# Performance work log

Hardware: AMD Instinct MI355X
Metric: run time of the kernel (lower is better)

## Reference

```python
import jax, jax.numpy as jnp
import numpy as np

B = 8            # batch
P = 28           # patch grid (224 / 8 for wide_resnet50_2 layer2)
D = 1536         # 512 (layer2) + 1024 (layer3) channels
M = 50000        # memory bank size
NUM_NEIGHBORS = 9
INPUT_SIZE = 224
SIGMA = 4.0
KSIZE = 2 * int(4.0 * SIGMA + 0.5) + 1  # 33, anomalib GaussianBlur2d convention


def setup_inputs() -> dict:
    key = jax.random.key(0)
    k1, k2 = jax.random.split(key)
    embedding = jax.random.normal(k1, (B * P * P, D), dtype=jnp.float32)
    memory_bank = jax.random.normal(k2, (M, D), dtype=jnp.float32)
    return {"embedding": embedding, "memory_bank": memory_bank}


def euclidean_dist(x, y):
    x_norm = jnp.sum(x * x, axis=-1, keepdims=True)
    y_norm = jnp.sum(y * y, axis=-1, keepdims=True)
    res = x_norm - 2.0 * jnp.matmul(x, jnp.swapaxes(y, -2, -1)) + jnp.swapaxes(y_norm, -2, -1)
    return jnp.sqrt(jnp.clip(res, 0.0, None))


def gaussian_kernel1d(ksize, sigma):
    x = jnp.arange(ksize, dtype=jnp.float32) - (ksize - 1) / 2.0
    g = jnp.exp(-(x * x) / (2.0 * sigma * sigma))
    return g / jnp.sum(g)


def gaussian_blur(img):
    # separable depthwise gaussian blur with reflect padding (kornia/anomalib style), img: [B,1,H,W]
    g = gaussian_kernel1d(KSIZE, SIGMA)
    pad = KSIZE // 2
    img = jnp.pad(img, ((0, 0), (0, 0), (pad, pad), (pad, pad)), mode='reflect')
    kh = g.reshape(1, 1, KSIZE, 1)
    kw = g.reshape(1, 1, 1, KSIZE)
    dn = ('NCHW', 'OIHW', 'NCHW')
    img = jax.lax.conv_general_dilated(img, kh, (1, 1), 'VALID', dimension_numbers=dn)
    img = jax.lax.conv_general_dilated(img, kw, (1, 1), 'VALID', dimension_numbers=dn)
    return img


def reference(embedding, memory_bank):
    # ---- nearest_neighbors(embedding, n_neighbors=1) ----
    dists = euclidean_dist(embedding, memory_bank)            # [B*P*P, M]
    patch_scores = jnp.min(dists, axis=1).reshape(B, P * P)   # [B, P*P]
    locations = jnp.argmin(dists, axis=1).reshape(B, P * P)   # [B, P*P]

    # ---- compute_anomaly_score (num_neighbors = 9) ----
    batch_idx = jnp.arange(B)
    max_patches = jnp.argmax(patch_scores, axis=1)                       # [B]
    feats = embedding.reshape(B, P * P, D)
    max_patches_features = feats[batch_idx, max_patches]                 # [B, D]
    score = patch_scores[batch_idx, max_patches]                         # [B]
    nn_index = locations[batch_idx, max_patches]                         # [B]
    nn_sample = memory_bank[nn_index]                                    # [B, D]
    d2 = euclidean_dist(nn_sample, memory_bank)                          # [B, M]
    _, support_samples = jax.lax.top_k(-d2, NUM_NEIGHBORS)               # smallest-k, ascending
    supp_feats = memory_bank[support_samples]                            # [B, K, D]
    d3 = euclidean_dist(max_patches_features[:, None, :], supp_feats)    # [B, 1, K]
    weights = (1.0 - jax.nn.softmax(d3[:, 0, :], axis=1))[:, 0]          # [B]
    pred_score = weights * score                                         # [B]

    # ---- anomaly map: bilinear upsample (align_corners=False) + gaussian blur ----
    pmap = patch_scores.reshape(B, 1, P, P)
    amap = jax.image.resize(pmap, (B, 1, INPUT_SIZE, INPUT_SIZE), method='bilinear')
    anomaly_map = gaussian_blur(amap)                                    # [B,1,224,224]
    return anomaly_map, pred_score
```

## Files before the change

kernel.cpp:

```cpp
#include <hip/hip_runtime.h>
#include <cstdint>
#include <cstddef>

#define DDIM 1536
#define NROWS 6272
#define NROWPAD 6400
#define MBANK 50000
#define NCOLPAD 50176
#define NRT 49
#define NCT 392
#define NSLOT (NCT * 2)
#define NKT 24
#define NB 8
#define PP 784
#define HW 224
#define KS 33
#define PAD 16

typedef __attribute__((ext_vector_type(4))) int int4v;
typedef __attribute__((ext_vector_type(4))) float floatx4;

__device__ __forceinline__ unsigned long long u64min(unsigned long long a, unsigned long long b) {
  return a < b ? a : b;
}

__global__ __launch_bounds__(256) void convnorm8_kernel(const float* __restrict__ in,
                                                        signed char* __restrict__ out,
                                                        float* __restrict__ norm,
                                                        int valid_rows, int total_rows) {
  int row = blockIdx.x * 4 + (threadIdx.x >> 6);
  int lane = threadIdx.x & 63;
  if (row >= total_rows) return;
  int* dst = (int*)(out + (size_t)row * DDIM);
  float s = 0.f;
  if (row < valid_rows) {
    const float4* src = (const float4*)(in + (size_t)row * DDIM);
#pragma unroll
    for (int i = 0; i < 6; i++) {
      int d = lane + i * 64;
      float4 v = src[d];
      s = fmaf(v.x, v.x, s); s = fmaf(v.y, v.y, s);
      s = fmaf(v.z, v.z, s); s = fmaf(v.w, v.w, s);
      int q0 = min(max((int)rintf(v.x * 16.f), -127), 127);
      int q1 = min(max((int)rintf(v.y * 16.f), -127), 127);
      int q2 = min(max((int)rintf(v.z * 16.f), -127), 127);
      int q3 = min(max((int)rintf(v.w * 16.f), -127), 127);
      dst[d] = (q0 & 255) | ((q1 & 255) << 8) | ((q2 & 255) << 16) | ((q3 & 255) << 24);
    }
  } else {
#pragma unroll
    for (int i = 0; i < 6; i++) dst[lane + i * 64] = 0;
  }
  for (int off = 32; off; off >>= 1) s += __shfl_down(s, off, 64);
  if (lane == 0) norm[row] = s;
}

__global__ __launch_bounds__(256) void rownorm_kernel(const float* __restrict__ x,
                                                      float* __restrict__ out, int rows) {
  int row = blockIdx.x;
  if (row >= rows) return;
  const float4* p4 = (const float4*)(x + (size_t)row * DDIM);
  float s = 0.f;
  for (int d = threadIdx.x; d < DDIM / 4; d += 256) {
    float4 v = p4[d];
    s = fmaf(v.x, v.x, s); s = fmaf(v.y, v.y, s);
    s = fmaf(v.z, v.z, s); s = fmaf(v.w, v.w, s);
  }
  for (int off = 32; off; off >>= 1) s += __shfl_down(s, off, 64);
  __shared__ float ls[4];
  int wid = threadIdx.x >> 6, lane = threadIdx.x & 63;
  if (lane == 0) ls[wid] = s;
  __syncthreads();
  if (threadIdx.x == 0) out[row] = ls[0] + ls[1] + ls[2] + ls[3];
}

__global__ void init_u64_kernel(unsigned long long* p, int n) {
  int i = blockIdx.x * 256 + threadIdx.x;
  if (i < n) p[i] = ~0ull;
}

__global__ __launch_bounds__(256, 4) void mindist_mfma_kernel(
    const signed char* __restrict__ Ah, const signed char* __restrict__ Bh,
    const float* __restrict__ xnorm, const float* __restrict__ ynorm,
    unsigned long long* __restrict__ cand) {
  __shared__ char smem[32768];

  const int t = threadIdx.x;
  const int lane = t & 63, wid = t >> 6;
  const int wm = wid >> 1, wn = wid & 1;
  const int l15 = lane & 15, g = lane >> 4;

  const int wg = (blockIdx.x & 7) * 2401 + (blockIdx.x >> 3);
  const int rt = wg / NCT, ct = wg % NCT;
  const int row0 = rt * 128;
  const int c0 = ct * 128;

  const int ck = ((g ^ ((l15 >> 1) & 3)) << 4);
  const int aBase = wm * 4096 + l15 * 64;
  const int bBase = 16384 + wn * 4096 + l15 * 64;

  const int cl = (t & 3) ^ ((t >> 3) & 3);
  const signed char* paBase = Ah + (size_t)(row0 + (t >> 2)) * DDIM + cl * 16;
  const signed char* pbBase = Bh + (size_t)(c0 + (t >> 2)) * DDIM + cl * 16;

#define STAGE_KT(kt, d)                                                                  \
  {                                                                                      \
    _Pragma("unroll") for (int j = 0; j < 2; j++) {                                      \
      __builtin_amdgcn_global_load_lds(                                                  \
          (const __attribute__((address_space(1))) void*)(paBase +                       \
              (size_t)(j * 64) * DDIM + (size_t)(kt) * 64),                              \
          (__attribute__((address_space(3))) void*)(smem + (d) * 8192 + j * 4096 +       \
                                                    wid * 1024),                         \
          16, 0, 0);                                                                     \
    }                                                                                    \
    _Pragma("unroll") for (int j = 0; j < 2; j++) {                                      \
      __builtin_amdgcn_global_load_lds(                                                  \
          (const __attribute__((address_space(1))) void*)(pbBase +                       \
              (size_t)(j * 64) * DDIM + (size_t)(kt) * 64),                              \
          (__attribute__((address_space(3))) void*)(smem + 16384 + (d) * 8192 +          \
                                                    j * 4096 + wid * 1024),              \
          16, 0, 0);                                                                     \
    }                                                                                    \
  }

  int4v acc[4][4];
  int4v zz = {0, 0, 0, 0};
#pragma unroll
  for (int mi = 0; mi < 4; mi++)
#pragma unroll
    for (int nf = 0; nf < 4; nf++) acc[mi][nf] = zz;

  STAGE_KT(0, 0);
  STAGE_KT(1, 1);

  for (int kt = 0; kt < NKT; ++kt) {
    const int d = kt & 1;
    if (kt < NKT - 1) {
      asm volatile("s_waitcnt vmcnt(4)" ::: "memory");
    } else {
      asm volatile("s_waitcnt vmcnt(0)" ::: "memory");
    }
    __builtin_amdgcn_sched_barrier(0);
    __builtin_amdgcn_s_barrier();
    __builtin_amdgcn_sched_barrier(0);

    const char* sA = smem + d * 8192 + aBase;
    const char* sB = smem + d * 8192 + bBase;

    int4v ra[4], rb[4];
#pragma unroll
    for (int mi = 0; mi < 4; mi++) ra[mi] = *(const int4v*)(sA + mi * 1024 + ck);
#pragma unroll
    for (int nf = 0; nf < 4; nf++) rb[nf] = *(const int4v*)(sB + nf * 1024 + ck);
    __builtin_amdgcn_s_setprio(1);
#pragma unroll
    for (int mi = 0; mi < 4; mi++)
#pragma unroll
      for (int nf = 0; nf < 4; nf++)
        acc[mi][nf] = __builtin_amdgcn_mfma_i32_16x16x64_i8(ra[mi], rb[nf],
                                                            acc[mi][nf], 0, 0, 0);
    __builtin_amdgcn_s_setprio(0);
    __builtin_amdgcn_sched_barrier(0);
    __builtin_amdgcn_s_barrier();
    __builtin_amdgcn_sched_barrier(0);
    if (kt < NKT - 2) STAGE_KT(kt + 2, d);
  }
#undef STAGE_KT

  float yn[4];
  int colv[4];
#pragma unroll
  for (int nf = 0; nf < 4; nf++) {
    int col = c0 + wn * 64 + nf * 16 + l15;
    colv[nf] = col;
    yn[nf] = (col < MBANK) ? ynorm[col] : 0.f;
  }
#pragma unroll
  for (int mi = 0; mi < 4; mi++) {
    int rowb = row0 + wm * 64 + mi * 16 + g * 4;
#pragma unroll
    for (int q = 0; q < 4; q++) {
      float xnq = xnorm[rowb + q];
      unsigned long long best = ~0ull;
#pragma unroll
      for (int nf = 0; nf < 4; nf++) {
        if (colv[nf] < MBANK) {
          float dsq = fmaxf(xnq + yn[nf] - (float)acc[mi][nf][q] * 0.0078125f, 0.f);
          unsigned long long pk =
              ((unsigned long long)__float_as_uint(dsq) << 32) | (unsigned)colv[nf];
          best = u64min(best, pk);
        }
      }
#pragma unroll
      for (int mask = 1; mask <= 8; mask <<= 1)
        best = u64min(best, __shfl_xor(best, mask, 64));
      if (l15 == 0 && rowb + q < NROWS)
        cand[(size_t)(rowb + q) * NSLOT + ct * 2 + wn] = best;
    }
  }
}

__global__ __launch_bounds__(256) void rerank_kernel(
    const float* __restrict__ emb, const float* __restrict__ mem,
    const float* __restrict__ xnorm, const float* __restrict__ ynorm,
    const unsigned long long* __restrict__ cand, float* __restrict__ ps,
    int* __restrict__ loc) {
  int row = blockIdx.x, t = threadIdx.x;
  int lane = t & 63, wave = t >> 6;
  __shared__ unsigned long long lred[4];
  __shared__ int glist[64];
  __shared__ int gcount;
  __shared__ float gmin;
  const unsigned long long* crow = cand + (size_t)row * NSLOT;
  unsigned long long mn = ~0ull;
  for (int i = t; i < NSLOT; i += 256) mn = u64min(mn, crow[i]);
  for (int off = 32; off; off >>= 1) {
    unsigned long long o = __shfl_down(mn, off, 64);
    mn = u64min(mn, o);
  }
  if (lane == 0) lred[wave] = mn;
  if (t == 0) gcount = 0;
  __syncthreads();
  if (t == 0) {
    unsigned long long m0 = lred[0];
    for (int w = 1; w < 4; w++) m0 = u64min(m0, lred[w]);
    gmin = __uint_as_float((unsigned)(m0 >> 32));
  }
  __syncthreads();
  float gate = gmin + 14.0f;
  for (int i = t; i < NSLOT; i += 256) {
    unsigned long long v = crow[i];
    float dq = __uint_as_float((unsigned)(v >> 32));
    if (dq <= gate) {
      int idx = atomicAdd(&gcount, 1);
      if (idx < 64) glist[idx] = (int)(v & 0xffffffffu);
    }
  }
  __syncthreads();
  int ng = min(gcount, 64);
  float xnv = xnorm[row];
  const float4* xp = (const float4*)(emb + (size_t)row * DDIM);
  unsigned long long best = ~0ull;
  for (int gi = wave; gi < ng; gi += 4) {
    int col = glist[gi];
    const float4* yp = (const float4*)(mem + (size_t)col * DDIM);
    float s = 0.f;
    for (int d4 = lane; d4 < DDIM / 4; d4 += 64) {
      float4 a = xp[d4], b = yp[d4];
      s = fmaf(a.x, b.x, s); s = fmaf(a.y, b.y, s);
      s = fmaf(a.z, b.z, s); s = fmaf(a.w, b.w, s);
    }
    for (int off = 32; off; off >>= 1) s += __shfl_down(s, off, 64);
    if (lane == 0) {
      float dsq = fmaxf(xnv + ynorm[col] - 2.f * s, 0.f);
      unsigned long long pk =
          ((unsigned long long)__float_as_uint(dsq) << 32) | (unsigned)col;
      best = u64min(best, pk);
    }
  }
  if (lane == 0) lred[wave] = best;
  __syncthreads();
  if (t == 0) {
    unsigned long long b = lred[0];
    for (int w = 1; w < 4; w++) b = u64min(b, lred[w]);
    ps[row] = sqrtf(__uint_as_float((unsigned)(b >> 32)));
    loc[row] = (int)(b & 0xffffffffu);
  }
}

#define BM 128
#define BN 128
#define DKC 16
#define FCSPLIT 16
#define FCT ((MBANK + BN - 1) / BN)
#define FCPB ((FCT + FCSPLIT - 1) / FCSPLIT)

__global__ __launch_bounds__(256) void mindist_kernel(
    const float* __restrict__ A, const float* __restrict__ Bm,
    const float* __restrict__ xnorm, const float* __restrict__ ynorm,
    unsigned long long* __restrict__ best) {
  __shared__ float Asf[DKC][BM];
  __shared__ float Bsf[DKC][BN];
  int t = threadIdx.x;
  int tx = t & 15, ty = t >> 4;
  int row0 = blockIdx.x * BM;
  int rloc[8], cloc[8];
#pragma unroll
  for (int i = 0; i < 4; i++) {
    rloc[i] = ty * 4 + i; rloc[i + 4] = 64 + ty * 4 + i;
    cloc[i] = tx * 4 + i; cloc[i + 4] = 64 + tx * 4 + i;
  }
  float xnv[8];
#pragma unroll
  for (int i = 0; i < 8; i++) xnv[i] = xnorm[row0 + rloc[i]];
  unsigned long long bestr[8];
#pragma unroll
  for (int i = 0; i < 8; i++) bestr[i] = ~0ull;
  int ct_begin = blockIdx.y * FCPB;
  int ct_end = ct_begin + FCPB; if (ct_end > FCT) ct_end = FCT;
  for (int ct = ct_begin; ct < ct_end; ++ct) {
    int c0 = ct * BN;
    float acc[8][8];
#pragma unroll
    for (int i = 0; i < 8; i++)
#pragma unroll
      for (int j = 0; j < 8; j++) acc[i][j] = 0.f;
    for (int dk = 0; dk < DDIM; dk += DKC) {
#pragma unroll
      for (int s = 0; s < 2; ++s) {
        int q = t + s * 256;
        int r = q >> 2, c4 = q & 3;
        float4 va = *(const float4*)(A + (size_t)(row0 + r) * DDIM + dk + c4 * 4);
        Asf[c4 * 4 + 0][r] = va.x; Asf[c4 * 4 + 1][r] = va.y;
        Asf[c4 * 4 + 2][r] = va.z; Asf[c4 * 4 + 3][r] = va.w;
        int col = c0 + r;
        float4 vb = make_float4(0.f, 0.f, 0.f, 0.f);
        if (col < MBANK) vb = *(const float4*)(Bm + (size_t)col * DDIM + dk + c4 * 4);
        Bsf[c4 * 4 + 0][r] = vb.x; Bsf[c4 * 4 + 1][r] = vb.y;
        Bsf[c4 * 4 + 2][r] = vb.z; Bsf[c4 * 4 + 3][r] = vb.w;
      }
      __syncthreads();
#pragma unroll
      for (int k = 0; k < DKC; k++) {
        float4 a0 = *(const float4*)&Asf[k][ty * 4];
        float4 a1 = *(const float4*)&Asf[k][64 + ty * 4];
        float4 b0 = *(const float4*)&Bsf[k][tx * 4];
        float4 b1 = *(const float4*)&Bsf[k][64 + tx * 4];
        float av[8] = {a0.x, a0.y, a0.z, a0.w, a1.x, a1.y, a1.z, a1.w};
        float bv[8] = {b0.x, b0.y, b0.z, b0.w, b1.x, b1.y, b1.z, b1.w};
#pragma unroll
        for (int i = 0; i < 8; i++)
#pragma unroll
          for (int j = 0; j < 8; j++) acc[i][j] = fmaf(av[i], bv[j], acc[i][j]);
      }
      __syncthreads();
    }
#pragma unroll
    for (int j = 0; j < 8; j++) {
      int col = c0 + cloc[j];
      if (col < MBANK) {
        float yn = ynorm[col];
#pragma unroll
        for (int i = 0; i < 8; i++) {
          float dsq = fmaxf(xnv[i] + yn - 2.f * acc[i][j], 0.f);
          unsigned long long pk =
              ((unsigned long long)__float_as_uint(dsq) << 32) | (unsigned)col;
          if (pk < bestr[i]) bestr[i] = pk;
        }
      }
    }
  }
#pragma unroll
  for (int i = 0; i < 8; i++) atomicMin(&best[row0 + rloc[i]], bestr[i]);
}

__global__ void unpack_kernel(const unsigned long long* __restrict__ best,
                              float* __restrict__ ps, int* __restrict__ loc) {
  int i = blockIdx.x * 256 + threadIdx.x;
  if (i >= NROWS) return;
  unsigned long long v = best[i];
  ps[i] = sqrtf(__uint_as_float((unsigned)(v >> 32)));
  loc[i] = (int)(v & 0xffffffffu);
}

__global__ __launch_bounds__(256) void argmax_kernel(const float* __restrict__ ps,
                                                     const int* __restrict__ loc,
                                                     float* __restrict__ bscore,
                                                     int* __restrict__ bfrow,
                                                     int* __restrict__ bnn) {
  int b = blockIdx.x, t = threadIdx.x;
  unsigned long long bp = 0;
  for (int p = t; p < PP; p += 256) {
    unsigned long long pk = ((unsigned long long)__float_as_uint(ps[b * PP + p]) << 32) |
                            (unsigned)(0xffffffffu - (unsigned)p);
    if (pk > bp) bp = pk;
  }
  for (int off = 32; off; off >>= 1) {
    unsigned long long o = __shfl_down(bp, off, 64);
    if (o > bp) bp = o;
  }
  __shared__ unsigned long long ls[4];
  int wid = t >> 6, lane = t & 63;
  if (lane == 0) ls[wid] = bp;
  __syncthreads();
  if (t == 0) {
    for (int w = 1; w < 4; w++) if (ls[w] > ls[0]) ls[0] = ls[w];
    unsigned p = 0xffffffffu - (unsigned)(ls[0] & 0xffffffffu);
    bscore[b] = __uint_as_float((unsigned)(ls[0] >> 32));
    bfrow[b] = b * PP + (int)p;
    bnn[b] = loc[b * PP + (int)p];
  }
}

__global__ __launch_bounds__(256) void d2_kernel(const float* __restrict__ mem,
                                                 const float* __restrict__ ynorm,
                                                 const int* __restrict__ bnn,
                                                 float* __restrict__ d2) {
  __shared__ float nn8[NB][DDIM];
  __shared__ float nnorm[NB];
  for (int e = threadIdx.x; e < NB * DDIM; e += 256) {
    int b = e / DDIM, d = e % DDIM;
    nn8[b][d] = mem[(size_t)bnn[b] * DDIM + d];
  }
  if (threadIdx.x < NB) nnorm[threadIdx.x] = ynorm[bnn[threadIdx.x]];
  __syncthreads();
  int wid = threadIdx.x >> 6, lane = threadIdx.x & 63;
  int gw = blockIdx.x * 4 + wid;
  int nw = gridDim.x * 4;
  for (int m = gw; m < MBANK; m += nw) {
    const float4* mp4 = (const float4*)(mem + (size_t)m * DDIM);
    float acc[NB];
#pragma unroll
    for (int b = 0; b < NB; b++) acc[b] = 0.f;
    for (int d4 = lane; d4 < DDIM / 4; d4 += 64) {
      float4 v = mp4[d4];
#pragma unroll
      for (int b = 0; b < NB; b++) {
        float4 w = *(const float4*)&nn8[b][d4 * 4];
        acc[b] = fmaf(v.x, w.x, acc[b]); acc[b] = fmaf(v.y, w.y, acc[b]);
        acc[b] = fmaf(v.z, w.z, acc[b]); acc[b] = fmaf(v.w, w.w, acc[b]);
      }
    }
    float yn = ynorm[m];
#pragma unroll
    for (int b = 0; b < NB; b++) {
      float r = acc[b];
      for (int off = 32; off; off >>= 1) r += __shfl_down(r, off, 64);
      if (lane == 0) d2[(size_t)b * MBANK + m] = sqrtf(fmaxf(nnorm[b] + yn - 2.f * r, 0.f));
    }
  }
}

__global__ __launch_bounds__(256) void topk_kernel(
    const float* __restrict__ emb, const float* __restrict__ mem,
    const float* __restrict__ xnorm, const float* __restrict__ ynorm,
    const float* __restrict__ d2, const float* __restrict__ bscore,
    const int* __restrict__ bfrow, float* __restrict__ pred) {
  int b = blockIdx.x, t = threadIdx.x;
  __shared__ unsigned long long ls9[256][9];
  __shared__ float fred[4];
  __shared__ int supp[9];
  __shared__ float d3s[9];
  const float* row = d2 + (size_t)b * MBANK;
  unsigned long long a0 = ~0ull, a1 = ~0ull, a2 = ~0ull, a3 = ~0ull, a4 = ~0ull,
                     a5 = ~0ull, a6 = ~0ull, a7 = ~0ull, a8 = ~0ull;
  for (int m = t; m < MBANK; m += 256) {
    unsigned long long pk = ((unsigned long long)__float_as_uint(row[m]) << 32) | (unsigned)m;
    if (pk < a8) {
      a8 = pk;
      unsigned long long tv;
#define CSWP(x, y) if (y < x) { tv = x; x = y; y = tv; }
      CSWP(a7, a8) CSWP(a6, a7) CSWP(a5, a6) CSWP(a4, a5)
      CSWP(a3, a4) CSWP(a2, a3) CSWP(a1, a2) CSWP(a0, a1)
#undef CSWP
    }
  }
  ls9[t][0] = a0; ls9[t][1] = a1; ls9[t][2] = a2; ls9[t][3] = a3; ls9[t][4] = a4;
  ls9[t][5] = a5; ls9[t][6] = a6; ls9[t][7] = a7; ls9[t][8] = a8;
  __syncthreads();
  for (int s = 128; s >= 1; s >>= 1) {
    if (t < s) {
      unsigned long long outv[9];
      int i = 0, j = 0;
#pragma unroll
      for (int k = 0; k < 9; k++) {
        unsigned long long x = ls9[t][i], y = ls9[t + s][j];
        if (x <= y) { outv[k] = x; i++; } else { outv[k] = y; j++; }
      }
#pragma unroll
      for (int k = 0; k < 9; k++) ls9[t][k] = outv[k];
    }
    __syncthreads();
  }
  if (t < 9) supp[t] = (int)(ls9[0][t] & 0xffffffffu);
  __syncthreads();
  int frow = bfrow[b];
  const float* x = emb + (size_t)frow * DDIM;
  float xnv = xnorm[frow];
  for (int k = 0; k < 9; k++) {
    const float* y = mem + (size_t)supp[k] * DDIM;
    float s = 0.f;
    for (int d = t; d < DDIM; d += 256) s = fmaf(x[d], y[d], s);
    for (int off = 32; off; off >>= 1) s += __shfl_down(s, off, 64);
    if ((t & 63) == 0) fred[t >> 6] = s;
    __syncthreads();
    if (t == 0) {
      float dot = fred[0] + fred[1] + fred[2] + fred[3];
      d3s[k] = sqrtf(fmaxf(xnv - 2.f * dot + ynorm[supp[k]], 0.f));
    }
    __syncthreads();
  }
  if (t == 0) {
    float mx = d3s[0];
    for (int k = 1; k < 9; k++) mx = fmaxf(mx, d3s[k]);
    float sum = 0.f;
    for (int k = 0; k < 9; k++) sum += expf(d3s[k] - mx);
    float w = 1.f - expf(d3s[0] - mx) / sum;
    pred[b] = w * bscore[b];
  }
}

__global__ void gauss_kernel(float* __restrict__ g) {
  __shared__ float tmp[KS];
  int t = threadIdx.x;
  if (t < KS) {
    float x = (float)t - (float)(KS - 1) * 0.5f;
    tmp[t] = __expf(-(x * x) / 32.0f);
  }
  __syncthreads();
  if (t == 0) {
    float s = 0.f;
    for (int j = 0; j < KS; j++) s += tmp[j];
    for (int j = 0; j < KS; j++) g[j] = tmp[j] / s;
  }
}

__global__ __launch_bounds__(256) void resize_kernel(const float* __restrict__ ps,
                                                     float* __restrict__ out) {
  int idx = blockIdx.x * 256 + threadIdx.x;
  if (idx >= NB * HW * HW) return;
  int x = idx % HW, y = (idx / HW) % HW, b = idx / (HW * HW);
  float sx = (x + 0.5f) * 0.125f - 0.5f;
  float sy = (y + 0.5f) * 0.125f - 0.5f;
  int x0 = (int)floorf(sx), y0 = (int)floorf(sy);
  float fx = sx - x0, fy = sy - y0;
  int x0c = min(max(x0, 0), 27), x1c = min(max(x0 + 1, 0), 27);
  int y0c = min(max(y0, 0), 27), y1c = min(max(y0 + 1, 0), 27);
  const float* p = ps + b * PP;
  float v00 = p[y0c * 28 + x0c], v01 = p[y0c * 28 + x1c];
  float v10 = p[y1c * 28 + x0c], v11 = p[y1c * 28 + x1c];
  out[idx] = v00 * (1.f - fy) * (1.f - fx) + v01 * (1.f - fy) * fx +
             v10 * fy * (1.f - fx) + v11 * fy * fx;
}

__device__ __forceinline__ int reflect224(int i) {
  if (i < 0) i = -i;
  if (i > 223) i = 446 - i;
  return i;
}

__global__ __launch_bounds__(256) void blurv_kernel(const float* __restrict__ in,
                                                    const float* __restrict__ g,
                                                    float* __restrict__ out) {
  __shared__ float gk[KS];
  if (threadIdx.x < KS) gk[threadIdx.x] = g[threadIdx.x];
  __syncthreads();
  int idx = blockIdx.x * 256 + threadIdx.x;
  if (idx >= NB * HW * HW) return;
  int x = idx % HW, y = (idx / HW) % HW, b = idx / (HW * HW);
  const float* base = in + (size_t)b * HW * HW;
  float s = 0.f;
#pragma unroll
  for (int j = 0; j < KS; j++) {
    int yy = reflect224(y - PAD + j);
    s = fmaf(gk[j], base[yy * HW + x], s);
  }
  out[idx] = s;
}

__global__ __launch_bounds__(256) void blurh_kernel(const float* __restrict__ in,
                                                    const float* __restrict__ g,
                                                    float* __restrict__ out) {
  __shared__ float gk[KS];
  if (threadIdx.x < KS) gk[threadIdx.x] = g[threadIdx.x];
  __syncthreads();
  int idx = blockIdx.x * 256 + threadIdx.x;
  if (idx >= NB * HW * HW) return;
  int x = idx % HW, y = (idx / HW) % HW, b = idx / (HW * HW);
  const float* base = in + (size_t)b * HW * HW;
  float s = 0.f;
#pragma unroll
  for (int j = 0; j < KS; j++) {
    int xx = reflect224(x - PAD + j);
    s = fmaf(gk[j], base[y * HW + xx], s);
  }
  out[idx] = s;
}

extern "C" void kernel_launch(void* const* d_in, const int* in_sizes, int n_in,
                              void* d_out, int out_size, void* d_ws, size_t ws_size,
                              hipStream_t stream) {
  const float* emb = (const float*)d_in[0];
  const float* mem = (const float*)d_in[1];
  float* out = (float*)d_out;

  char* ws = (char*)d_ws;
  size_t off = 0;
  auto alloc = [&](size_t bytes) -> void* {
    void* p = ws + off;
    off += (bytes + 255) & ~(size_t)255;
    return p;
  };
  float* ynorm = (float*)alloc((size_t)NCOLPAD * 4);
  float* xnorm = (float*)alloc((size_t)NROWPAD * 4);
  unsigned long long* cand =
      (unsigned long long*)alloc((size_t)NROWS * NSLOT * 8);
  float* ps = (float*)alloc(NROWS * 4);
  int* loc = (int*)alloc(NROWS * 4);
  float* bscore = (float*)alloc(NB * 4);
  int* bfrow = (int*)alloc(NB * 4);
  int* bnn = (int*)alloc(NB * 4);
  float* d2 = (float*)alloc((size_t)NB * MBANK * 4);
  float* g = (float*)alloc(KS * 4);
  float* rsz = (float*)alloc((size_t)NB * HW * HW * 4);
  float* tmp = (float*)alloc((size_t)NB * HW * HW * 4);
  signed char* emb_q = (signed char*)alloc((size_t)NROWPAD * DDIM);
  signed char* mem_q = (signed char*)alloc((size_t)NCOLPAD * DDIM);
  size_t full_need = off;

  bool fast = (ws_size >= full_need);

  if (fast) {
    convnorm8_kernel<<<NCOLPAD / 4, 256, 0, stream>>>(mem, mem_q, ynorm, MBANK, NCOLPAD);
    convnorm8_kernel<<<NROWPAD / 4, 256, 0, stream>>>(emb, emb_q, xnorm, NROWS, NROWPAD);
    mindist_mfma_kernel<<<NRT * NCT, 256, 0, stream>>>(emb_q, mem_q, xnorm, ynorm, cand);
    rerank_kernel<<<NROWS, 256, 0, stream>>>(emb, mem, xnorm, ynorm, cand, ps, loc);
    argmax_kernel<<<NB, 256, 0, stream>>>(ps, loc, bscore, bfrow, bnn);
  } else {
    rownorm_kernel<<<MBANK, 256, 0, stream>>>(mem, ynorm, MBANK);
    rownorm_kernel<<<NROWS, 256, 0, stream>>>(emb, xnorm, NROWS);
    unsigned long long* best = cand;
    init_u64_kernel<<<(NROWS + 255) / 256, 256, 0, stream>>>(best, NROWS);
    mindist_kernel<<<dim3(NROWS / BM, FCSPLIT), 256, 0, stream>>>(emb, mem, xnorm, ynorm,
                                                                  best);
    unpack_kernel<<<(NROWS + 255) / 256, 256, 0, stream>>>(best, ps, loc);
    argmax_kernel<<<NB, 256, 0, stream>>>(ps, loc, bscore, bfrow, bnn);
  }

  d2_kernel<<<1200, 256, 0, stream>>>(mem, ynorm, bnn, d2);
  topk_kernel<<<NB, 256, 0, stream>>>(emb, mem, xnorm, ynorm, d2, bscore, bfrow,
                                      out + (size_t)NB * HW * HW);
  gauss_kernel<<<1, 64, 0, stream>>>(g);
  resize_kernel<<<(NB * HW * HW + 255) / 256, 256, 0, stream>>>(ps, rsz);
  blurv_kernel<<<(NB * HW * HW + 255) / 256, 256, 0, stream>>>(rsz, g, tmp);
  blurh_kernel<<<(NB * HW * HW + 255) / 256, 256, 0, stream>>>(tmp, g, out);
}
```

Baseline: 1.012 ms.

## Fold resize and blur into a 224x28 linear operator; merge conversion kernels

Replaces the bilinear resize and the two separable blur passes with one precomputed 224x28 weight matrix that combines interpolation, reflect padding and the Gaussian. Each batch image is then produced as W·P·Wᵀ by a single block working in shared memory. This removes three full-resolution intermediate passes and several launches. The memory-bank and embedding int8 conversion kernels are also merged into a single launch. The trade-off is only 8 blocks for the anomaly map, so little GPU parallelism, with a serial wprep kernel ahead of it.

```diff
diff --git a/kernel.cpp b/kernel.cpp
--- a/kernel.cpp
+++ b/kernel.cpp
@@ -24,21 +24,44 @@
   return a < b ? a : b;
 }
 
-__global__ __launch_bounds__(256) void convnorm8_kernel(const float* __restrict__ in,
-                                                        signed char* __restrict__ out,
-                                                        float* __restrict__ norm,
-                                                        int valid_rows, int total_rows) {
+__device__ __forceinline__ int reflect224(int i) {
+  if (i < 0) i = -i;
+  if (i > 223) i = 446 - i;
+  return i;
+}
+
+__global__ __launch_bounds__(256) void convnorm_both_kernel(
+    const float* __restrict__ mem, const float* __restrict__ emb,
+    signed char* __restrict__ mem_q, signed char* __restrict__ emb_q,
+    float* __restrict__ ynorm, float* __restrict__ xnorm) {
   int row = blockIdx.x * 4 + (threadIdx.x >> 6);
   int lane = threadIdx.x & 63;
-  if (row >= total_rows) return;
-  int* dst = (int*)(out + (size_t)row * DDIM);
+  const float* src;
+  int* dst;
+  float* norm;
+  bool valid;
+  int r;
+  if (row < NCOLPAD) {
+    r = row;
+    src = mem + (size_t)r * DDIM;
+    dst = (int*)(mem_q + (size_t)r * DDIM);
+    norm = ynorm + r;
+    valid = (r < MBANK);
+  } else {
+    r = row - NCOLPAD;
+    if (r >= NROWPAD) return;
+    src = emb + (size_t)r * DDIM;
+    dst = (int*)(emb_q + (size_t)r * DDIM);
+    norm = xnorm + r;
+    valid = (r < NROWS);
+  }
   float s = 0.f;
-  if (row < valid_rows) {
-    const float4* src = (const float4*)(in + (size_t)row * DDIM);
+  if (valid) {
+    const float4* s4 = (const float4*)src;
 #pragma unroll
     for (int i = 0; i < 6; i++) {
       int d = lane + i * 64;
-      float4 v = src[d];
+      float4 v = s4[d];
       s = fmaf(v.x, v.x, s); s = fmaf(v.y, v.y, s);
       s = fmaf(v.z, v.z, s); s = fmaf(v.w, v.w, s);
       int q0 = min(max((int)rintf(v.x * 16.f), -127), 127);
@@ -52,7 +75,7 @@
     for (int i = 0; i < 6; i++) dst[lane + i * 64] = 0;
   }
   for (int off = 32; off; off >>= 1) s += __shfl_down(s, off, 64);
-  if (lane == 0) norm[row] = s;
+  if (lane == 0) *norm = s;
 }
 
 __global__ __launch_bounds__(256) void rownorm_kernel(const float* __restrict__ x,
@@ -500,81 +523,58 @@
   }
 }
 
-__global__ void gauss_kernel(float* __restrict__ g) {
-  __shared__ float tmp[KS];
-  int t = threadIdx.x;
-  if (t < KS) {
-    float x = (float)t - (float)(KS - 1) * 0.5f;
-    tmp[t] = __expf(-(x * x) / 32.0f);
-  }
-  __syncthreads();
-  if (t == 0) {
+__global__ __launch_bounds__(256) void wprep_kernel(float* __restrict__ W) {
+  int y = threadIdx.x;
+  if (y >= HW) return;
+  float sum = 0.f;
+  for (int j = 0; j < KS; j++) {
+    float xj = (float)j - (float)(KS - 1) * 0.5f;
+    sum += __expf(-(xj * xj) / 32.0f);
+  }
+  float inv = 1.f / sum;
+  for (int r = 0; r < 28; r++) {
+    float w = 0.f;
+    for (int j = 0; j < KS; j++) {
+      float xj = (float)j - (float)(KS - 1) * 0.5f;
+      float gj = __expf(-(xj * xj) / 32.0f) * inv;
+      int v = reflect224(y - PAD + j);
+      float sy = (v + 0.5f) * 0.125f - 0.5f;
+      int y0 = (int)floorf(sy);
+      float fy = sy - y0;
+      int r0 = min(max(y0, 0), 27), r1 = min(max(y0 + 1, 0), 27);
+      float u = (r == r0 ? (1.f - fy) : 0.f) + (r == r1 ? fy : 0.f);
+      w = fmaf(gj, u, w);
+    }
+    W[y * 28 + r] = w;
+  }
+}
+
+__global__ __launch_bounds__(256) void anomap_kernel(const float* __restrict__ ps,
+                                                     const float* __restrict__ W,
+                                                     float* __restrict__ out) {
+  __shared__ float Ps[28 * 28];
+  __shared__ float Ws[HW * 28];
+  __shared__ float Ts[28 * HW];
+  int b = blockIdx.x, t = threadIdx.x;
+  for (int i = t; i < 28 * 28; i += 256) Ps[i] = ps[b * PP + i];
+  for (int i = t; i < HW * 28; i += 256) Ws[i] = W[i];
+  __syncthreads();
+  for (int i = t; i < 28 * HW; i += 256) {
+    int r = i / HW, x = i % HW;
     float s = 0.f;
-    for (int j = 0; j < KS; j++) s += tmp[j];
-    for (int j = 0; j < KS; j++) g[j] = tmp[j] / s;
-  }
-}
-
-__global__ __launch_bounds__(256) void resize_kernel(const float* __restrict__ ps,
-                                                     float* __restrict__ out) {
-  int idx = blockIdx.x * 256 + threadIdx.x;
-  if (idx >= NB * HW * HW) return;
-  int x = idx % HW, y = (idx / HW) % HW, b = idx / (HW * HW);
-  float sx = (x + 0.5f) * 0.125f - 0.5f;
-  float sy = (y + 0.5f) * 0.125f - 0.5f;
-  int x0 = (int)floorf(sx), y0 = (int)floorf(sy);
-  float fx = sx - x0, fy = sy - y0;
-  int x0c = min(max(x0, 0), 27), x1c = min(max(x0 + 1, 0), 27);
-  int y0c = min(max(y0, 0), 27), y1c = min(max(y0 + 1, 0), 27);
-  const float* p = ps + b * PP;
-  float v00 = p[y0c * 28 + x0c], v01 = p[y0c * 28 + x1c];
-  float v10 = p[y1c * 28 + x0c], v11 = p[y1c * 28 + x1c];
-  out[idx] = v00 * (1.f - fy) * (1.f - fx) + v01 * (1.f - fy) * fx +
-             v10 * fy * (1.f - fx) + v11 * fy * fx;
-}
-
-__device__ __forceinline__ int reflect224(int i) {
-  if (i < 0) i = -i;
-  if (i > 223) i = 446 - i;
-  return i;
-}
-
-__global__ __launch_bounds__(256) void blurv_kernel(const float* __restrict__ in,
-                                                    const float* __restrict__ g,
-                                                    float* __restrict__ out) {
-  __shared__ float gk[KS];
-  if (threadIdx.x < KS) gk[threadIdx.x] = g[threadIdx.x];
-  __syncthreads();
-  int idx = blockIdx.x * 256 + threadIdx.x;
-  if (idx >= NB * HW * HW) return;
-  int x = idx % HW, y = (idx / HW) % HW, b = idx / (HW * HW);
-  const float* base = in + (size_t)b * HW * HW;
-  float s = 0.f;
-#pragma unroll
-  for (int j = 0; j < KS; j++) {
-    int yy = reflect224(y - PAD + j);
-    s = fmaf(gk[j], base[yy * HW + x], s);
-  }
-  out[idx] = s;
-}
-
-__global__ __launch_bounds__(256) void blurh_kernel(const float* __restrict__ in,
-                                                    const float* __restrict__ g,
-                                                    float* __restrict__ out) {
-  __shared__ float gk[KS];
-  if (threadIdx.x < KS) gk[threadIdx.x] = g[threadIdx.x];
-  __syncthreads();
-  int idx = blockIdx.x * 256 + threadIdx.x;
-  if (idx >= NB * HW * HW) return;
-  int x = idx % HW, y = (idx / HW) % HW, b = idx / (HW * HW);
-  const float* base = in + (size_t)b * HW * HW;
-  float s = 0.f;
-#pragma unroll
-  for (int j = 0; j < KS; j++) {
-    int xx = reflect224(x - PAD + j);
-    s = fmaf(gk[j], base[y * HW + xx], s);
-  }
-  out[idx] = s;
+#pragma unroll
+    for (int c = 0; c < 28; c++) s = fmaf(Ps[r * 28 + c], Ws[x * 28 + c], s);
+    Ts[r * HW + x] = s;
+  }
+  __syncthreads();
+  float* ob = out + (size_t)b * HW * HW;
+  for (int i = t; i < HW * HW; i += 256) {
+    int y = i / HW, x = i % HW;
+    float s = 0.f;
+#pragma unroll
+    for (int r = 0; r < 28; r++) s = fmaf(Ws[y * 28 + r], Ts[r * HW + x], s);
+    ob[i] = s;
+  }
 }
 
 extern "C" void kernel_launch(void* const* d_in, const int* in_sizes, int n_in,
@@ -601,9 +601,7 @@
   int* bfrow = (int*)alloc(NB * 4);
   int* bnn = (int*)alloc(NB * 4);
   float* d2 = (float*)alloc((size_t)NB * MBANK * 4);
-  float* g = (float*)alloc(KS * 4);
-  float* rsz = (float*)alloc((size_t)NB * HW * HW * 4);
-  float* tmp = (float*)alloc((size_t)NB * HW * HW * 4);
+  float* W = (float*)alloc((size_t)HW * 28 * 4);
   signed char* emb_q = (signed char*)alloc((size_t)NROWPAD * DDIM);
   signed char* mem_q = (signed char*)alloc((size_t)NCOLPAD * DDIM);
   size_t full_need = off;
@@ -611,8 +609,8 @@
   bool fast = (ws_size >= full_need);
 
   if (fast) {
-    convnorm8_kernel<<<NCOLPAD / 4, 256, 0, stream>>>(mem, mem_q, ynorm, MBANK, NCOLPAD);
-    convnorm8_kernel<<<NROWPAD / 4, 256, 0, stream>>>(emb, emb_q, xnorm, NROWS, NROWPAD);
+    convnorm_both_kernel<<<(NCOLPAD + NROWPAD) / 4, 256, 0, stream>>>(mem, emb, mem_q,
+                                                                      emb_q, ynorm, xnorm);
     mindist_mfma_kernel<<<NRT * NCT, 256, 0, stream>>>(emb_q, mem_q, xnorm, ynorm, cand);
     rerank_kernel<<<NROWS, 256, 0, stream>>>(emb, mem, xnorm, ynorm, cand, ps, loc);
     argmax_kernel<<<NB, 256, 0, stream>>>(ps, loc, bscore, bfrow, bnn);
@@ -630,8 +628,6 @@
   d2_kernel<<<1200, 256, 0, stream>>>(mem, ynorm, bnn, d2);
   topk_kernel<<<NB, 256, 0, stream>>>(emb, mem, xnorm, ynorm, d2, bscore, bfrow,
                                       out + (size_t)NB * HW * HW);
-  gauss_kernel<<<1, 64, 0, stream>>>(g);
-  resize_kernel<<<(NB * HW * HW + 255) / 256, 256, 0, stream>>>(ps, rsz);
-  blurv_kernel<<<(NB * HW * HW + 255) / 256, 256, 0, stream>>>(rsz, g, tmp);
-  blurh_kernel<<<(NB * HW * HW + 255) / 256, 256, 0, stream>>>(tmp, g, out);
-}
+  wprep_kernel<<<1, 256, 0, stream>>>(W);
+  anomap_kernel<<<NB, 256, 0, stream>>>(ps, W, out);
+}
```

After: 1.142 ms. 1.13x slower.
